# Performance work log

Hardware: AMD Instinct MI355X
Metric: run time of the kernel (lower is better)

## Reference

```python
import jax, jax.numpy as jnp
import numpy as np

B, N, H, W, P = 32, 6, 512, 512, 512
SCALE, ASPECT, MIN_PH = 0.5, 1.0, 60.0


def setup_inputs() -> dict:
    key = jax.random.key(0)
    k1, k2, k3, k4, k5, k6 = jax.random.split(key, 6)
    images = jax.random.normal(k1, (B, H, W, 3), jnp.float32)
    patch = jax.random.normal(k2, (P, P, 3), jnp.float32)
    # person bboxes (ymin, xmin, ymax, xmax) in pixels, fully inside the image
    hsz = jax.random.uniform(k3, (B, N), jnp.float32, 120.0, 400.0)
    wsz = jax.random.uniform(k4, (B, N), jnp.float32, 120.0, 400.0)
    ymin = jax.random.uniform(k5, (B, N), jnp.float32) * (H - hsz)
    xmin = jax.random.uniform(k6, (B, N), jnp.float32) * (W - wsz)
    boxes = jnp.stack([ymin, xmin, ymin + hsz, xmin + wsz], axis=-1)
    return {"images": images, "boxes": boxes, "patch": patch}


def _patch_boxes(boxes):
    # Patcher.create: derive (ymin_patch, xmin_patch, patch_h, patch_w) from each bbox
    ymin, xmin, ymax, xmax = (boxes[..., 0], boxes[..., 1], boxes[..., 2], boxes[..., 3])
    h = ymax - ymin
    w = xmax - xmin
    pw = h * SCALE
    ph = ASPECT * pw
    oy = ymin + h * 0.5
    ox = xmin + w * 0.5
    yp = jnp.maximum(oy - ph * 0.5, 0.0)
    xp = jnp.maximum(ox - pw * 0.5, 0.0)
    yp = jnp.where(yp + ph > H, H - ph, yp)
    xp = jnp.where(xp + pw > W, W - pw, xp)
    valid = ph > MIN_PH  # ragged filter -> mask
    return jnp.stack([yp, xp, ph, pw], axis=-1), valid


def _paste_one(img, patch, box, valid):
    # fused gather(resize bilinear, half-pixel centers) + scatter of the patch into img
    Pn = patch.shape[0]
    b = box.astype(jnp.int32)  # tf.cast truncation
    y0b, x0b, h, w = b[0], b[1], b[2], b[3]
    hf = jnp.maximum(h, 1).astype(jnp.float32)
    wf = jnp.maximum(w, 1).astype(jnp.float32)
    dy = jnp.arange(img.shape[0]) - y0b
    dx = jnp.arange(img.shape[1]) - x0b
    sy = jnp.clip((dy.astype(jnp.float32) + 0.5) * (Pn / hf) - 0.5, 0.0, Pn - 1.0)
    sx = jnp.clip((dx.astype(jnp.float32) + 0.5) * (Pn / wf) - 0.5, 0.0, Pn - 1.0)
    yl = jnp.floor(sy).astype(jnp.int32); yh = jnp.minimum(yl + 1, Pn - 1); wy = sy - yl
    xl = jnp.floor(sx).astype(jnp.int32); xh = jnp.minimum(xl + 1, Pn - 1); wx = sx - xl
    # separable bilinear: rows [H, P, 3] then cols -> [H, W, 3]
    rows = patch[yl] * (1.0 - wy)[:, None, None] + patch[yh] * wy[:, None, None]
    val = rows[:, xl] * (1.0 - wx)[None, :, None] + rows[:, xh] * wx[None, :, None]
    inside = ((dy >= 0) & (dy < h))[:, None] & ((dx >= 0) & (dx < w))[None, :] & valid
    return jnp.where(inside[..., None], val, img)


def reference(images, boxes, patch):
    pboxes, valid = _patch_boxes(boxes)
    def step(imgs, xs):
        bx, v = xs  # [B,4], [B]
        imgs = jax.vmap(lambda im, b_, v_: _paste_one(im, patch, b_, v_))(imgs, bx, v)
        return imgs, None
    # sequential over patches (later patches overwrite earlier, as in the tf while_loop)
    out, _ = jax.lax.scan(step, images, (jnp.transpose(pboxes, (1, 0, 2)), valid.T))
    return out
```

## Files before the change

### kernel.cpp

```cpp
#include <hip/hip_runtime.h>


#define Nn 6
#define Hh 512
#define Ww 512
#define Pp 512

typedef float v4f __attribute__((ext_vector_type(4)));

__global__ __launch_bounds__(256) void patch_attack_kernel(
    const float* __restrict__ images,
    const float* __restrict__ boxes,
    const float* __restrict__ patch,
    float* __restrict__ out)
{
    __shared__ int   s_y0[Nn], s_x0[Nn], s_h[Nn], s_w[Nn];
    __shared__ float s_sy[Nn], s_sx[Nn];
    __shared__ float s_res[256 * 3];
    __shared__ unsigned char s_cov[256];

    const int tid = threadIdx.x;
    const int b = blockIdx.x >> 10;

    if (tid < Nn) {
        const int n = tid;
        const float* bx = boxes + ((size_t)b * Nn + n) * 4;
        const float ymin = bx[0], xmin = bx[1], ymax = bx[2], xmax = bx[3];
        const float h  = ymax - ymin;
        const float w  = xmax - xmin;
        const float pw = h * 0.5f;
        const float ph = pw;
        const float oy = ymin + h * 0.5f;
        const float ox = xmin + w * 0.5f;
        float yp = fmaxf(oy - ph * 0.5f, 0.0f);
        float xp = fmaxf(ox - pw * 0.5f, 0.0f);
        yp = (yp + ph > 512.0f) ? (512.0f - ph) : yp;
        xp = (xp + pw > 512.0f) ? (512.0f - pw) : xp;
        const bool valid = ph > 60.0f;
        const int hI = (int)ph;
        const int wI = (int)pw;
        s_y0[n] = (int)yp;
        s_x0[n] = (int)xp;
        s_h[n]  = valid ? hI : 0;
        s_w[n]  = wI;
        s_sy[n] = 512.0f / (float)(hI > 1 ? hI : 1);
        s_sx[n] = 512.0f / (float)(wI > 1 ? wI : 1);
    }
    __syncthreads();

    const int pix = blockIdx.x * 256 + tid;
    const int rem = pix & (Hh * Ww - 1);
    const int y   = rem >> 9;
    const int x   = rem & (Ww - 1);

    float r0 = 0.0f, r1 = 0.0f, r2 = 0.0f;
    bool covered = false;

    #pragma unroll
    for (int n = Nn - 1; n >= 0; --n) {
        const int dy = y - s_y0[n];
        const int dx = x - s_x0[n];
        if ((unsigned)dy < (unsigned)s_h[n] && (unsigned)dx < (unsigned)s_w[n]) {
            float sy = ((float)dy + 0.5f) * s_sy[n] - 0.5f;
            float sx = ((float)dx + 0.5f) * s_sx[n] - 0.5f;
            sy = fminf(fmaxf(sy, 0.0f), 511.0f);
            sx = fminf(fmaxf(sx, 0.0f), 511.0f);
            const int yl = (int)sy;
            const int yh = (yl + 1 < 511) ? (yl + 1) : 511;
            const float wy = sy - (float)yl;
            const int xl = (int)sx;
            const int xh = (xl + 1 < 511) ? (xl + 1) : 511;
            const float wx = sx - (float)xl;
            const float omwy = 1.0f - wy;
            const float omwx = 1.0f - wx;

            const float* __restrict__ pll = patch + ((size_t)yl * Pp + xl) * 3;
            const float* __restrict__ plh = patch + ((size_t)yl * Pp + xh) * 3;
            const float* __restrict__ phl = patch + ((size_t)yh * Pp + xl) * 3;
            const float* __restrict__ phh = patch + ((size_t)yh * Pp + xh) * 3;
            r0 = (pll[0] * omwy + phl[0] * wy) * omwx + (plh[0] * omwy + phh[0] * wy) * wx;
            r1 = (pll[1] * omwy + phl[1] * wy) * omwx + (plh[1] * omwy + phh[1] * wy) * wx;
            r2 = (pll[2] * omwy + phl[2] * wy) * omwx + (plh[2] * omwy + phh[2] * wy) * wx;
            covered = true;
            break;
        }
    }

    s_res[tid * 3 + 0] = r0;
    s_res[tid * 3 + 1] = r1;
    s_res[tid * 3 + 2] = r2;
    s_cov[tid] = covered ? 1 : 0;
    __syncthreads();

    if (tid < 192) {
        const int f0 = tid << 2;
        const size_t gf = (size_t)blockIdx.x * 768 + f0;
        const bool c0 = s_cov[(f0 + 0) / 3];
        const bool c1 = s_cov[(f0 + 1) / 3];
        const bool c2 = s_cov[(f0 + 2) / 3];
        const bool c3 = s_cov[(f0 + 3) / 3];
        v4f v = {0.0f, 0.0f, 0.0f, 0.0f};
        if (!(c0 && c1 && c2 && c3)) {
            v = __builtin_nontemporal_load((const v4f*)(images + gf));
        }
        v4f o;
        o.x = c0 ? s_res[f0 + 0] : v.x;
        o.y = c1 ? s_res[f0 + 1] : v.y;
        o.z = c2 ? s_res[f0 + 2] : v.z;
        o.w = c3 ? s_res[f0 + 3] : v.w;
        __builtin_nontemporal_store(o, (v4f*)(out + gf));
    }
}

extern "C" void kernel_launch(void* const* d_in, const int* in_sizes, int n_in,
                              void* d_out, int out_size, void* d_ws, size_t ws_size,
                              hipStream_t stream) {
    const float* images = (const float*)d_in[0];
    const float* boxes  = (const float*)d_in[1];
    const float* patch  = (const float*)d_in[2];
    float* out = (float*)d_out;

    const int total_pixels = 32 * Hh * Ww;
    const int block = 256;
    const int grid  = total_pixels / block;

    patch_attack_kernel<<<grid, block, 0, stream>>>(images, boxes, patch, out);
}
```

Before: 190.7 us.

## Process one image row per block with per-row y-interpolation hoisted

Each block now handles a full image row of 384 threads, each owning one float4 of interleaved RGB. The vertical bilinear terms (row offsets, wy) and the row-hit test are computed once per box per row in shared memory, so per-pixel work is only the x interpolation. The shared-memory staging, the second barrier and the 192/256 idle-thread write phase are removed. The image is now loaded unconditionally even when fully covered, and each thread does per-channel patch loads for 4 floats, which may cost extra scattered gathers.

```diff
diff --git a/kernel.cpp b/kernel.cpp
--- a/kernel.cpp
+++ b/kernel.cpp
@@ -2,25 +2,24 @@
 
 
 #define Nn 6
-#define Hh 512
-#define Ww 512
 #define Pp 512
 
 typedef float v4f __attribute__((ext_vector_type(4)));
 
-__global__ __launch_bounds__(256) void patch_attack_kernel(
+__global__ __launch_bounds__(384) void patch_attack_kernel(
     const float* __restrict__ images,
     const float* __restrict__ boxes,
     const float* __restrict__ patch,
     float* __restrict__ out)
 {
-    __shared__ int   s_y0[Nn], s_x0[Nn], s_h[Nn], s_w[Nn];
-    __shared__ float s_sy[Nn], s_sx[Nn];
-    __shared__ float s_res[256 * 3];
-    __shared__ unsigned char s_cov[256];
+    __shared__ int      s_x0[Nn], s_offl[Nn], s_offh[Nn];
+    __shared__ unsigned s_w[Nn];
+    __shared__ float    s_sx[Nn], s_wy[Nn], s_omwy[Nn];
 
+    const int row = blockIdx.x;
+    const int b   = row >> 9;
+    const int y   = row & 511;
     const int tid = threadIdx.x;
-    const int b = blockIdx.x >> 10;
 
     if (tid < Nn) {
         const int n = tid;
@@ -39,77 +38,67 @@
         const bool valid = ph > 60.0f;
         const int hI = (int)ph;
         const int wI = (int)pw;
-        s_y0[n] = (int)yp;
+        const int y0 = (int)yp;
+        const int dy = y - y0;
+        const bool rowhit = valid && (unsigned)dy < (unsigned)hI;
+        s_w[n]  = rowhit ? (unsigned)wI : 0u;
         s_x0[n] = (int)xp;
-        s_h[n]  = valid ? hI : 0;
-        s_w[n]  = wI;
-        s_sy[n] = 512.0f / (float)(hI > 1 ? hI : 1);
         s_sx[n] = 512.0f / (float)(wI > 1 ? wI : 1);
+        const float sys = 512.0f / (float)(hI > 1 ? hI : 1);
+        float sy = ((float)dy + 0.5f) * sys - 0.5f;
+        sy = fminf(fmaxf(sy, 0.0f), 511.0f);
+        const int yl = (int)sy;
+        const int yh = (yl + 1 < 511) ? (yl + 1) : 511;
+        s_wy[n]   = sy - (float)yl;
+        s_omwy[n] = 1.0f - s_wy[n];
+        s_offl[n] = yl * (Pp * 3);
+        s_offh[n] = yh * (Pp * 3);
     }
     __syncthreads();
 
-    const int pix = blockIdx.x * 256 + tid;
-    const int rem = pix & (Hh * Ww - 1);
-    const int y   = rem >> 9;
-    const int x   = rem & (Ww - 1);
+    const int f0 = tid << 2;
+    const size_t g = (size_t)row * 1536 + f0;
+    v4f img = __builtin_nontemporal_load((const v4f*)(images + g));
 
-    float r0 = 0.0f, r1 = 0.0f, r2 = 0.0f;
-    bool covered = false;
-
+    unsigned w_[Nn]; int x0_[Nn], offl_[Nn], offh_[Nn];
+    float sx_[Nn], wy_[Nn], omwy_[Nn];
     #pragma unroll
-    for (int n = Nn - 1; n >= 0; --n) {
-        const int dy = y - s_y0[n];
-        const int dx = x - s_x0[n];
-        if ((unsigned)dy < (unsigned)s_h[n] && (unsigned)dx < (unsigned)s_w[n]) {
-            float sy = ((float)dy + 0.5f) * s_sy[n] - 0.5f;
-            float sx = ((float)dx + 0.5f) * s_sx[n] - 0.5f;
-            sy = fminf(fmaxf(sy, 0.0f), 511.0f);
-            sx = fminf(fmaxf(sx, 0.0f), 511.0f);
-            const int yl = (int)sy;
-            const int yh = (yl + 1 < 511) ? (yl + 1) : 511;
-            const float wy = sy - (float)yl;
-            const int xl = (int)sx;
-            const int xh = (xl + 1 < 511) ? (xl + 1) : 511;
-            const float wx = sx - (float)xl;
-            const float omwy = 1.0f - wy;
-            const float omwx = 1.0f - wx;
-
-            const float* __restrict__ pll = patch + ((size_t)yl * Pp + xl) * 3;
-            const float* __restrict__ plh = patch + ((size_t)yl * Pp + xh) * 3;
-            const float* __restrict__ phl = patch + ((size_t)yh * Pp + xl) * 3;
-            const float* __restrict__ phh = patch + ((size_t)yh * Pp + xh) * 3;
-            r0 = (pll[0] * omwy + phl[0] * wy) * omwx + (plh[0] * omwy + phh[0] * wy) * wx;
-            r1 = (pll[1] * omwy + phl[1] * wy) * omwx + (plh[1] * omwy + phh[1] * wy) * wx;
-            r2 = (pll[2] * omwy + phl[2] * wy) * omwx + (plh[2] * omwy + phh[2] * wy) * wx;
-            covered = true;
-            break;
-        }
+    for (int n = 0; n < Nn; ++n) {
+        w_[n] = s_w[n];   x0_[n] = s_x0[n];
+        offl_[n] = s_offl[n]; offh_[n] = s_offh[n];
+        sx_[n] = s_sx[n]; wy_[n] = s_wy[n]; omwy_[n] = s_omwy[n];
     }
 
-    s_res[tid * 3 + 0] = r0;
-    s_res[tid * 3 + 1] = r1;
-    s_res[tid * 3 + 2] = r2;
-    s_cov[tid] = covered ? 1 : 0;
-    __syncthreads();
+    float res[4];
+    #pragma unroll
+    for (int j = 0; j < 4; ++j) {
+        const int f  = f0 + j;
+        const int px = f / 3;
+        const int c  = f - px * 3;
+        float v = img[j];
+        #pragma unroll
+        for (int n = Nn - 1; n >= 0; --n) {
+            const int dx = px - x0_[n];
+            if ((unsigned)dx < w_[n]) {
+                float sx = ((float)dx + 0.5f) * sx_[n] - 0.5f;
+                sx = fminf(fmaxf(sx, 0.0f), 511.0f);
+                const int xl = (int)sx;
+                const int xh = (xl + 1 < 511) ? (xl + 1) : 511;
+                const float wx   = sx - (float)xl;
+                const float omwx = 1.0f - wx;
+                const float* __restrict__ rl = patch + offl_[n];
+                const float* __restrict__ rh = patch + offh_[n];
+                const int al = xl * 3 + c, ah = xh * 3 + c;
+                v = (rl[al] * omwy_[n] + rh[al] * wy_[n]) * omwx
+                  + (rl[ah] * omwy_[n] + rh[ah] * wy_[n]) * wx;
+                break;
+            }
+        }
+        res[j] = v;
+    }
 
-    if (tid < 192) {
-        const int f0 = tid << 2;
-        const size_t gf = (size_t)blockIdx.x * 768 + f0;
-        const bool c0 = s_cov[(f0 + 0) / 3];
-        const bool c1 = s_cov[(f0 + 1) / 3];
-        const bool c2 = s_cov[(f0 + 2) / 3];
-        const bool c3 = s_cov[(f0 + 3) / 3];
-        v4f v = {0.0f, 0.0f, 0.0f, 0.0f};
-        if (!(c0 && c1 && c2 && c3)) {
-            v = __builtin_nontemporal_load((const v4f*)(images + gf));
-        }
-        v4f o;
-        o.x = c0 ? s_res[f0 + 0] : v.x;
-        o.y = c1 ? s_res[f0 + 1] : v.y;
-        o.z = c2 ? s_res[f0 + 2] : v.z;
-        o.w = c3 ? s_res[f0 + 3] : v.w;
-        __builtin_nontemporal_store(o, (v4f*)(out + gf));
-    }
+    v4f o = {res[0], res[1], res[2], res[3]};
+    __builtin_nontemporal_store(o, (v4f*)(out + g));
 }
 
 extern "C" void kernel_launch(void* const* d_in, const int* in_sizes, int n_in,
@@ -120,9 +109,6 @@
     const float* patch  = (const float*)d_in[2];
     float* out = (float*)d_out;
 
-    const int total_pixels = 32 * Hh * Ww;
-    const int block = 256;
-    const int grid  = total_pixels / block;
-
-    patch_attack_kernel<<<grid, block, 0, stream>>>(images, boxes, patch, out);
+    const int rows = 32 * 512;
+    patch_attack_kernel<<<rows, 384, 0, stream>>>(images, boxes, patch, out);
 }
```

Measured after the change: 202.0 us. 1.06x slower.
